# Optimization experiments

Measured on AMD Instinct MI355X. Metric: run time of the kernel, lower is better.

## Reference

```python
import jax, jax.numpy as jnp
import numpy as np

# Config constants (match init_kwargs)
E = 32          # num_experts
K = 4           # num_experts_per_token
G = 4           # num_expert_group
TG = 2          # topk_group
H = 2048        # hidden_size
F = 1024        # moe_intermediate_size
FS = 2048       # shared expert intermediate (moe_intermediate_size * num_shared_experts)
SCALE = 2.0     # routed_scaling_factor
B, S = 2, 1024
N = B * S
CAP = 2 * (N * K // E)


def setup_inputs() -> dict:
    key = jax.random.key(0)
    ks = jax.random.split(key, 9)
    w = 0.02  # init scale for weights
    return {
        "hidden_states": jax.random.normal(ks[0], (B, S, H), jnp.float32),
        "gate_w": jax.random.normal(ks[1], (E, H), jnp.float32) * w,
        "gate_bias": jax.random.normal(ks[2], (E,), jnp.float32) * w,
        "w1": jax.random.normal(ks[3], (E, H, F), jnp.float32) * w,
        "w2": jax.random.normal(ks[4], (E, F, H), jnp.float32) * w,
        "w3": jax.random.normal(ks[5], (E, H, F), jnp.float32) * w,
        "shared_gate": jax.random.normal(ks[6], (H, FS), jnp.float32) * w,
        "shared_up": jax.random.normal(ks[7], (H, FS), jnp.float32) * w,
        "shared_down": jax.random.normal(ks[8], (FS, H), jnp.float32) * w,
    }


def _gate(x, gate_w, gate_bias):
    # x: [N, H] -> (topk_idx [N,K] int32, topk_w [N,K] f32)
    logits = x @ gate_w.T                       # [N, E]
    scores = jax.nn.sigmoid(logits)
    sc = scores + gate_bias                     # scores_for_choice
    n = x.shape[0]
    grp = sc.reshape(n, G, E // G)
    group_scores = jax.lax.top_k(grp, 2)[0].sum(-1)          # [N, G]
    _, gidx = jax.lax.top_k(group_scores, TG)                # [N, TG]
    gmask = jnp.zeros((n, G), sc.dtype).at[jnp.arange(n)[:, None], gidx].set(1.0)
    smask = jnp.repeat(gmask, E // G, axis=1)                # [N, E]
    tmp = jnp.where(smask > 0, sc, 0.0)
    _, topk_idx = jax.lax.top_k(tmp, K)                      # [N, K]
    topk_w = jnp.take_along_axis(scores, topk_idx, axis=1)
    topk_w = topk_w / (topk_w.sum(-1, keepdims=True) + 1e-20)  # renormalize (K>1)
    return topk_idx, topk_w * SCALE


def _moe(x, topk_idx, topk_w, w1, w2, w3):
    # Capacity-based dispatch -> grouped SwiGLU GEMMs -> weighted combine.
    n = x.shape[0]
    flat_e = topk_idx.reshape(-1)                            # [N*K]
    oh = jax.nn.one_hot(flat_e, E, dtype=jnp.int32)
    pos = (jnp.cumsum(oh, axis=0) * oh).sum(-1) - 1          # slot within expert
    keep = pos < CAP
    slot = jnp.where(keep, pos, CAP)                         # CAP -> dropped via mode='drop'
    x_rep = jnp.repeat(x, K, axis=0)                         # [N*K, H]
    buf = jnp.zeros((E, CAP, H), x.dtype).at[flat_e, slot].set(x_rep, mode='drop')
    h = jax.nn.silu(jnp.einsum('ech,ehf->ecf', buf, w1)) * jnp.einsum('ech,ehf->ecf', buf, w3)
    ob = jnp.einsum('ecf,efh->ech', h, w2)                   # [E, CAP, H]
    y = ob[flat_e, jnp.minimum(slot, CAP - 1)]               # [N*K, H]
    y = jnp.where(keep[:, None], y, 0.0)
    return (y.reshape(n, K, H) * topk_w[:, :, None]).sum(1)  # [N, H]


def reference(hidden_states, gate_w, gate_bias, w1, w2, w3, shared_gate, shared_up, shared_down):
    b, s, h = hidden_states.shape
    x = hidden_states.reshape(-1, h)
    topk_idx, topk_w = _gate(x, gate_w, gate_bias)
    out = _moe(x, topk_idx, topk_w, w1, w2, w3)
    shared = (jax.nn.silu(x @ shared_gate) * (x @ shared_up)) @ shared_down
    return (out + shared).reshape(b, s, h)
```

## Files before the change

### kernel.cpp

```cpp
#include <hip/hip_runtime.h>
#include <stdint.h>
#include <math.h>

#define NTOK 2048
#define HDIM 2048
#define FDIM 1024
#define NEXP 32
#define TOPK 4
#define NGRP 4
#define CAP  512

typedef _Float16 f16;
typedef _Float16 half8 __attribute__((ext_vector_type(8)));
typedef float f32x4 __attribute__((ext_vector_type(4)));

__device__ __forceinline__ int swz3(int n) { return (n ^ (n >> 2)) & 3; }

__global__ __launch_bounds__(256) void gateconv_kernel(const float* __restrict__ x,
                                                       const float* __restrict__ gw,
                                                       const float* __restrict__ gb,
                                                       int* __restrict__ tidx,
                                                       float* __restrict__ tw,
                                                       f16* __restrict__ xbt) {
  int t = blockIdx.x;
  int tid = threadIdx.x;
  int e = tid >> 3, p = tid & 7;
  const f32x4* xr = (const f32x4*)(x + (size_t)t * HDIM);
  const f32x4* wr = (const f32x4*)(gw + (size_t)e * HDIM);
  float s = 0.f;
  for (int c = 0; c < 64; c++) {
    f32x4 a = xr[p + c * 8], w = wr[p + c * 8];
    s += a[0] * w[0] + a[1] * w[1] + a[2] * w[2] + a[3] * w[3];
  }
  s += __shfl_down(s, 4, 8);
  s += __shfl_down(s, 2, 8);
  s += __shfl_down(s, 1, 8);
  __shared__ float lg[NEXP];
  if (p == 0) lg[e] = s;

  {
    int c8 = tid * 8;
    const float* pp = x + (size_t)t * HDIM + c8;
    f32x4 a = *(const f32x4*)pp;
    f32x4 b = *(const f32x4*)(pp + 4);
    half8 v;
    v[0] = (f16)a[0]; v[1] = (f16)a[1]; v[2] = (f16)a[2]; v[3] = (f16)a[3];
    v[4] = (f16)b[0]; v[5] = (f16)b[1]; v[6] = (f16)b[2]; v[7] = (f16)b[3];
    *(half8*)((char*)xbt + (size_t)(c8 >> 5) * 131072 + t * 64 + (c8 & 31) * 2) = v;
  }

  __syncthreads();
  if (tid == 0) {
    float sc[NEXP], scb[NEXP];
    for (int i = 0; i < NEXP; i++) {
      sc[i] = 1.f / (1.f + expf(-lg[i]));
      scb[i] = sc[i] + gb[i];
    }
    float gs[NGRP];
    for (int g = 0; g < NGRP; g++) {
      float m1 = -1e30f, m2 = -1e30f;
      for (int j = 0; j < 8; j++) {
        float v = scb[g * 8 + j];
        if (v > m1) { m2 = m1; m1 = v; }
        else if (v > m2) m2 = v;
      }
      gs[g] = m1 + m2;
    }
    int g1 = 0; float bv = gs[0];
    for (int g = 1; g < NGRP; g++) if (gs[g] > bv) { bv = gs[g]; g1 = g; }
    int g2 = -1; bv = -1e30f;
    for (int g = 0; g < NGRP; g++) if (g != g1 && gs[g] > bv) { bv = gs[g]; g2 = g; }
    float cand[NEXP];
    for (int i = 0; i < NEXP; i++) {
      int g = i >> 3;
      cand[i] = (g == g1 || g == g2) ? scb[i] : 0.0f;
    }
    int isel[TOPK]; float wsel[TOPK]; float wsum = 0.f;
    bool used[NEXP] = {};
    for (int k = 0; k < TOPK; k++) {
      int best = 0; float bw = -1e30f;
      for (int i = 0; i < NEXP; i++)
        if (!used[i] && cand[i] > bw) { bw = cand[i]; best = i; }
      used[best] = true;
      isel[k] = best;
      wsel[k] = sc[best];
      wsum += wsel[k];
    }
    float inv = 2.0f / (wsum + 1e-20f);
    for (int k = 0; k < TOPK; k++) {
      tidx[t * TOPK + k] = isel[k];
      tw[t * TOPK + k] = wsel[k] * inv;
    }
  }
}

__global__ __launch_bounds__(256) void dispatch_kernel(const int* __restrict__ tidx,
                                                       const float* __restrict__ tw,
                                                       int* __restrict__ tok,
                                                       float* __restrict__ wt,
                                                       int* __restrict__ cnt) {
  int e = blockIdx.x, tid = threadIdx.x, wv = tid >> 6, lane = tid & 63;
  __shared__ int wsum[4];
  __shared__ int sbase;
  if (tid == 0) sbase = 0;
  __syncthreads();
  for (int c = 0; c < (NTOK * TOPK) / 256; c++) {
    int i = c * 256 + tid;
    int fe = tidx[i];
    bool flag = (fe == e);
    unsigned long long b = __ballot(flag ? 1 : 0);
    int lr = __popcll(b & ((1ull << lane) - 1ull));
    if (lane == 0) wsum[wv] = __popcll(b);
    __syncthreads();
    int off = 0;
    for (int w2 = 0; w2 < wv; w2++) off += wsum[w2];
    int tot = wsum[0] + wsum[1] + wsum[2] + wsum[3];
    int base = sbase;
    if (flag) {
      int pos = base + off + lr;
      if (pos < CAP) {
        tok[e * CAP + pos] = i >> 2;
        wt[e * CAP + pos] = tw[i];
      }
    }
    __syncthreads();
    if (tid == 0) sbase = base + tot;
  }
  __syncthreads();
  if (tid == 0) cnt[e] = min(sbase, CAP);
}

__global__ __launch_bounds__(256) void gather_kernel(const f16* __restrict__ xbt,
                                                     const int* __restrict__ tok,
                                                     const int* __restrict__ cnt,
                                                     f16* __restrict__ xg) {
  int bid = blockIdx.x;
  int t = bid & 63, e = bid >> 6;
  int cn = cnt[e];
  int tid = threadIdx.x;
  char* dst = (char*)xg + (size_t)e * 2097152 + (size_t)t * 32768;
  const char* srcb = (const char*)xbt + (size_t)t * 131072;
  for (int s = tid; s < cn; s += 256) {
    const uint4* sp = (const uint4*)(srcb + (size_t)tok[e * CAP + s] * 64);
    uint4 v0 = sp[0], v1 = sp[1], v2 = sp[2], v3 = sp[3];
    uint4* dp = (uint4*)(dst + s * 64);
    dp[0] = v0; dp[1] = v1; dp[2] = v2; dp[3] = v3;
  }
}

template<int MODE>
__device__ void gemm_body(int bid, const f16* __restrict__ Ag, const float* __restrict__ B0g,
                          const float* __restrict__ B1g, void* __restrict__ outp,
                          const int* __restrict__ tokL, const float* __restrict__ wtL,
                          const int* __restrict__ cntP, char* bs) {
  constexpr int BM = (MODE == 0 || MODE == 2) ? 512 : 256;
  constexpr int BN = (MODE == 2) ? 64 : 32;
  constexpr bool DUAL = (MODE <= 1);
  constexpr int MF = BM / 64;
  constexpr int NF = BN / 16;
  constexpr int KD = (MODE == 2) ? 1024 : 2048;
  constexpr int NK = KD / 32;
  constexpr int ND = (MODE == 0) ? 1024 : 2048;
  constexpr size_t TS = (MODE == 0 || MODE == 2) ? 32768 : 131072;
  constexpr int BSZ = (DUAL ? 2 : 1) * BN * 64;

  int tid = threadIdx.x, lane = tid & 63, wv = tid >> 6;
  int e = 0, m0 = 0, n0 = 0;
  if constexpr (MODE == 0 || MODE == 2) {
    e = (bid & 7) + ((bid >> 3) >> 5) * 8;
    n0 = ((bid >> 3) & 31) * BN;
  } else {
    n0 = ((bid & 7) * 8 + ((bid >> 3) & 7)) * 32;
    m0 = ((bid >> 3) >> 3) * 256;
  }

  const char* Ab = (const char*)Ag;
  const float* B0 = B0g;
  const float* B1 = B1g;
  int Mcur = 0;
  if constexpr (MODE == 0 || MODE == 2) {
    Mcur = cntP[e];
    Ab += (size_t)e * ((MODE == 0) ? 2097152 : 1048576);
    B0 += (size_t)e * ((size_t)KD * ND);
    if constexpr (MODE == 0) B1 += (size_t)e * ((size_t)KD * ND);
  }

  int kb = tid >> 3;
  int nbL = (tid & 7) * (BN / 8);

  unsigned voff[MF];
#pragma unroll
  for (int mf = 0; mf < MF; mf++) {
    int row = ((MODE == 0 || MODE == 2) ? (wv * (BM / 4)) : (m0 + wv * 64)) + mf * 16 + (lane & 15);
    voff[mf] = row * 64 + ((lane >> 4) << 4);
  }

  f32x4 acc0[MF][NF];
  f32x4 acc1[DUAL ? MF : 1][DUAL ? NF : 1];
#pragma unroll
  for (int mf = 0; mf < MF; mf++)
#pragma unroll
    for (int nf = 0; nf < NF; nf++) acc0[mf][nf] = (f32x4){0.f, 0.f, 0.f, 0.f};
  if constexpr (DUAL) {
#pragma unroll
    for (int mf = 0; mf < MF; mf++)
#pragma unroll
      for (int nf = 0; nf < NF; nf++) acc1[mf][nf] = (f32x4){0.f, 0.f, 0.f, 0.f};
  }

  half8 af[MF];
  half8 bf0[NF];
  half8 bf1[DUAL ? NF : 1];
  f32x4 bE0, bE1, bO0, bO1;

  auto loadB = [&](int t, f32x4& X, f32x4& Y) {
    const float* s = B0 + (size_t)(t * 32 + kb) * ND + n0 + nbL;
    X = *(const f32x4*)s;
    if constexpr (DUAL) {
      Y = *(const f32x4*)(B1 + (size_t)(t * 32 + kb) * ND + n0 + nbL);
    } else if constexpr (MODE == 2) {
      Y = *(const f32x4*)(s + 4);
    }
  };
  auto writeB = [&](const f32x4& X, const f32x4& Y, int par) {
    char* base = bs + par * BSZ;
#pragma unroll
    for (int q = 0; q < 4; q++) {
      int n = nbL + q;
      int off = n * 64 + (((kb >> 3) ^ swz3(n)) << 4) + (kb & 7) * 2;
      *(f16*)(base + off) = (f16)X[q];
      if constexpr (DUAL) {
        *(f16*)(base + BN * 64 + off) = (f16)Y[q];
      } else if constexpr (MODE == 2) {
        int n2 = n + 4;
        int off2 = n2 * 64 + (((kb >> 3) ^ swz3(n2)) << 4) + (kb & 7) * 2;
        *(f16*)(base + off2) = (f16)Y[q];
      }
    }
  };
  auto bfread = [&](int par) {
#pragma unroll
    for (int nf = 0; nf < NF; nf++) {
      int n = nf * 16 + (lane & 15);
      int off = par * BSZ + n * 64 + (((lane >> 4) ^ swz3(n)) << 4);
      bf0[nf] = *(const half8*)(bs + off);
      if constexpr (DUAL) bf1[nf] = *(const half8*)(bs + BN * 64 + off);
    }
  };
  auto loadAf = [&](int t) {
#pragma unroll
    for (int mf = 0; mf < MF; mf++)
      af[mf] = *(const half8*)(Ab + (size_t)t * TS + voff[mf]);
  };
  auto domfma = [&]() {
#pragma unroll
    for (int mf = 0; mf < MF; mf++)
#pragma unroll
      for (int nf = 0; nf < NF; nf++) {
        acc0[mf][nf] = __builtin_amdgcn_mfma_f32_16x16x32_f16(af[mf], bf0[nf], acc0[mf][nf], 0, 0, 0);
        if constexpr (DUAL)
          acc1[mf][nf] = __builtin_amdgcn_mfma_f32_16x16x32_f16(af[mf], bf1[nf], acc1[mf][nf], 0, 0, 0);
      }
  };

  loadB(0, bE0, bE1);
  loadB(1, bO0, bO1);
  loadAf(0);
  writeB(bE0, bE1, 0);
  asm volatile("s_waitcnt lgkmcnt(0)" ::: "memory");
  __builtin_amdgcn_s_barrier();

  for (int t = 0; t < NK; t += 2) {
    bfread(0);
    writeB(bO0, bO1, 1);
    if (t + 2 < NK) loadB(t + 2, bE0, bE1);
    domfma();
    loadAf(t + 1 < NK ? t + 1 : t);
    asm volatile("s_waitcnt lgkmcnt(0)" ::: "memory");
    __builtin_amdgcn_s_barrier();
    bfread(1);
    if (t + 2 < NK) writeB(bE0, bE1, 0);
    if (t + 3 < NK) loadB(t + 3, bO0, bO1);
    domfma();
    if (t + 2 < NK) {
      loadAf(t + 2);
      asm volatile("s_waitcnt lgkmcnt(0)" ::: "memory");
      __builtin_amdgcn_s_barrier();
    }
  }

  int koff = (lane >> 4) << 2;
  if constexpr (MODE == 0) {
    char* Hb = (char*)outp + (size_t)e * 1048576;
#pragma unroll
    for (int mf = 0; mf < MF; mf++)
#pragma unroll
      for (int j = 0; j < 4; j++) {
        int slot = wv * 128 + mf * 16 + koff + j;
        if (slot < Mcur) {
#pragma unroll
          for (int nf = 0; nf < NF; nf++) {
            int col = n0 + nf * 16 + (lane & 15);
            float g = acc0[mf][nf][j], u = acc1[mf][nf][j];
            float val = g / (1.f + expf(-g)) * u;
            *(f16*)(Hb + (size_t)(col >> 5) * 32768 + slot * 64 + (col & 31) * 2) = (f16)val;
          }
        }
      }
  } else if constexpr (MODE == 1) {
    char* Hb = (char*)outp;
#pragma unroll
    for (int mf = 0; mf < MF; mf++)
#pragma unroll
      for (int j = 0; j < 4; j++) {
        int row = m0 + wv * 64 + mf * 16 + koff + j;
#pragma unroll
        for (int nf = 0; nf < NF; nf++) {
          int col = n0 + nf * 16 + (lane & 15);
          float g = acc0[mf][nf][j], u = acc1[mf][nf][j];
          float val = g / (1.f + expf(-g)) * u;
          *(f16*)(Hb + (size_t)(col >> 5) * 131072 + row * 64 + (col & 31) * 2) = (f16)val;
        }
      }
  } else if constexpr (MODE == 2) {
    float* Of = (float*)outp;
    const int* tokp = tokL + e * CAP;
    const float* wtp = wtL + e * CAP;
#pragma unroll
    for (int mf = 0; mf < MF; mf++)
#pragma unroll
      for (int j = 0; j < 4; j++) {
        int slot = wv * 128 + mf * 16 + koff + j;
        if (slot < Mcur) {
          int tk = tokp[slot];
          float w = wtp[slot];
#pragma unroll
          for (int nf = 0; nf < NF; nf++) {
            int col = n0 + nf * 16 + (lane & 15);
            atomicAdd(Of + (size_t)tk * HDIM + col, acc0[mf][nf][j] * w);
          }
        }
      }
  } else {
    float* Of = (float*)outp;
#pragma unroll
    for (int mf = 0; mf < MF; mf++)
#pragma unroll
      for (int j = 0; j < 4; j++) {
        int row = m0 + wv * 64 + mf * 16 + koff + j;
#pragma unroll
        for (int nf = 0; nf < NF; nf++) {
          int col = n0 + nf * 16 + (lane & 15);
          atomicAdd(Of + (size_t)row * HDIM + col, acc0[mf][nf][j]);
        }
      }
  }
}

__global__ __launch_bounds__(256, 2) void fused_up_kernel(
    const f16* __restrict__ xg, const f16* __restrict__ xbt,
    const float* __restrict__ w1, const float* __restrict__ w3,
    const float* __restrict__ sg, const float* __restrict__ su,
    void* __restrict__ hbuf, void* __restrict__ hs, const int* __restrict__ cnt) {
  __shared__ __align__(16) char bs[8192];
  int bid = blockIdx.x;
  if (bid < 1024) gemm_body<0>(bid, xg, w1, w3, hbuf, nullptr, nullptr, cnt, bs);
  else            gemm_body<1>(bid - 1024, xbt, sg, su, hs, nullptr, nullptr, nullptr, bs);
}

__global__ __launch_bounds__(256, 2) void fused_down_kernel(
    const f16* __restrict__ hbuf, const f16* __restrict__ hs,
    const float* __restrict__ w2, const float* __restrict__ sd,
    float* __restrict__ out, const int* __restrict__ tok,
    const float* __restrict__ wt, const int* __restrict__ cnt) {
  __shared__ __align__(16) char bs[8192];
  int bid = blockIdx.x;
  if (bid < 1024) gemm_body<2>(bid, hbuf, w2, nullptr, out, tok, wt, cnt, bs);
  else            gemm_body<3>(bid - 1024, hs, sd, nullptr, out, nullptr, nullptr, nullptr, bs);
}

extern "C" void kernel_launch(void* const* d_in, const int* in_sizes, int n_in,
                              void* d_out, int out_size, void* d_ws, size_t ws_size,
                              hipStream_t stream) {
  const float* x  = (const float*)d_in[0];
  const float* gw = (const float*)d_in[1];
  const float* gb = (const float*)d_in[2];
  const float* w1 = (const float*)d_in[3];
  const float* w2 = (const float*)d_in[4];
  const float* w3 = (const float*)d_in[5];
  const float* sg = (const float*)d_in[6];
  const float* su = (const float*)d_in[7];
  const float* sd = (const float*)d_in[8];
  float* out = (float*)d_out;
  char* ws = (char*)d_ws;

  f16*   xbt = (f16*)(ws);
  f16*   hs  = (f16*)(ws + 8388608);
  f16*   hbuf= (f16*)(ws + 16777216);
  f16*   xg  = (f16*)(ws + 50331648);
  int*   tok = (int*)(ws + 117440512);
  float* wt  = (float*)(ws + 117506048);
  int*   tidx= (int*)(ws + 117571584);
  float* tw  = (float*)(ws + 117604352);
  int*   cnt = (int*)(ws + 117637120);

  gateconv_kernel<<<2048, 256, 0, stream>>>(x, gw, gb, tidx, tw, xbt);
  dispatch_kernel<<<32, 256, 0, stream>>>(tidx, tw, tok, wt, cnt);
  gather_kernel<<<2048, 256, 0, stream>>>(xbt, tok, cnt, xg);

  fused_up_kernel<<<1536, 256, 0, stream>>>(xg, xbt, w1, w3, sg, su, hbuf, hs, cnt);

  hipMemsetAsync(out, 0, (size_t)out_size * sizeof(float), stream);
  fused_down_kernel<<<1536, 256, 0, stream>>>(hbuf, hs, w2, sd, out, tok, wt, cnt);
}
```

Baseline: 545.4 us.

## Switch to 128x128 square GEMM tiles with compact expert packing and separate SwiGLU pass

Replaces the tall-skinny per-expert GEMM tiles (512x32/64) with a shared 128x128 core using a 2x2 wave layout. The goal is to raise reuse of both A and B per block and to cut redundant fp32 weight loads. Expert rows are now packed compactly through a prefix-sum offset kernel, and empty M tiles return early. The gate and up projections are written separately to fp16 buffers and combined by a new elementwise SwiGLU kernel, which adds extra memory traffic and two launches in exchange for the tiling change.

Result: no change. 548.9 us (+0.6%).

```diff
diff --git a/kernel.cpp b/kernel.cpp
--- a/kernel.cpp
+++ b/kernel.cpp
@@ -12,6 +12,7 @@
 
 typedef _Float16 f16;
 typedef _Float16 half8 __attribute__((ext_vector_type(8)));
+typedef _Float16 half2v __attribute__((ext_vector_type(2)));
 typedef float f32x4 __attribute__((ext_vector_type(4)));
 
 __device__ __forceinline__ int swz3(int n) { return (n ^ (n >> 2)) & 3; }
@@ -130,15 +131,23 @@
   if (tid == 0) cnt[e] = min(sbase, CAP);
 }
 
+__global__ void scan_kernel(const int* __restrict__ cnt, int* __restrict__ offs) {
+  if (threadIdx.x == 0) {
+    int s = 0;
+    for (int e = 0; e < NEXP; e++) { offs[e] = s; s += cnt[e]; }
+  }
+}
+
 __global__ __launch_bounds__(256) void gather_kernel(const f16* __restrict__ xbt,
                                                      const int* __restrict__ tok,
                                                      const int* __restrict__ cnt,
+                                                     const int* __restrict__ offs,
                                                      f16* __restrict__ xg) {
   int bid = blockIdx.x;
   int t = bid & 63, e = bid >> 6;
   int cn = cnt[e];
   int tid = threadIdx.x;
-  char* dst = (char*)xg + (size_t)e * 2097152 + (size_t)t * 32768;
+  char* dst = (char*)xg + (size_t)offs[e] * 4096 + (size_t)t * cn * 64;
   const char* srcb = (const char*)xbt + (size_t)t * 131072;
   for (int s = tid; s < cn; s += 256) {
     const uint4* sp = (const uint4*)(srcb + (size_t)tok[e * CAP + s] * 64);
@@ -148,235 +157,235 @@
   }
 }
 
-template<int MODE>
-__device__ void gemm_body(int bid, const f16* __restrict__ Ag, const float* __restrict__ B0g,
-                          const float* __restrict__ B1g, void* __restrict__ outp,
-                          const int* __restrict__ tokL, const float* __restrict__ wtL,
-                          const int* __restrict__ cntP, char* bs) {
-  constexpr int BM = (MODE == 0 || MODE == 2) ? 512 : 256;
-  constexpr int BN = (MODE == 2) ? 64 : 32;
-  constexpr bool DUAL = (MODE <= 1);
-  constexpr int MF = BM / 64;
-  constexpr int NF = BN / 16;
-  constexpr int KD = (MODE == 2) ? 1024 : 2048;
-  constexpr int NK = KD / 32;
-  constexpr int ND = (MODE == 0) ? 1024 : 2048;
-  constexpr size_t TS = (MODE == 0 || MODE == 2) ? 32768 : 131072;
-  constexpr int BSZ = (DUAL ? 2 : 1) * BN * 64;
-
+#define SYNC() { asm volatile("s_waitcnt lgkmcnt(0)" ::: "memory"); __builtin_amdgcn_s_barrier(); }
+
+__device__ __forceinline__ void core128(const char* __restrict__ Ab, int tsA, int NKt,
+                                        const float* __restrict__ Bb, int ND,
+                                        char* lds, f32x4 (&acc)[4][4]) {
   int tid = threadIdx.x, lane = tid & 63, wv = tid >> 6;
-  int e = 0, m0 = 0, n0 = 0;
-  if constexpr (MODE == 0 || MODE == 2) {
-    e = (bid & 7) + ((bid >> 3) >> 5) * 8;
-    n0 = ((bid >> 3) & 31) * BN;
-  } else {
-    n0 = ((bid & 7) * 8 + ((bid >> 3) & 7)) * 32;
-    m0 = ((bid >> 3) >> 3) * 256;
-  }
-
-  const char* Ab = (const char*)Ag;
-  const float* B0 = B0g;
-  const float* B1 = B1g;
-  int Mcur = 0;
-  if constexpr (MODE == 0 || MODE == 2) {
-    Mcur = cntP[e];
-    Ab += (size_t)e * ((MODE == 0) ? 2097152 : 1048576);
-    B0 += (size_t)e * ((size_t)KD * ND);
-    if constexpr (MODE == 0) B1 += (size_t)e * ((size_t)KD * ND);
-  }
-
-  int kb = tid >> 3;
-  int nbL = (tid & 7) * (BN / 8);
-
-  unsigned voff[MF];
-#pragma unroll
-  for (int mf = 0; mf < MF; mf++) {
-    int row = ((MODE == 0 || MODE == 2) ? (wv * (BM / 4)) : (m0 + wv * 64)) + mf * 16 + (lane & 15);
-    voff[mf] = row * 64 + ((lane >> 4) << 4);
-  }
-
-  f32x4 acc0[MF][NF];
-  f32x4 acc1[DUAL ? MF : 1][DUAL ? NF : 1];
-#pragma unroll
-  for (int mf = 0; mf < MF; mf++)
-#pragma unroll
-    for (int nf = 0; nf < NF; nf++) acc0[mf][nf] = (f32x4){0.f, 0.f, 0.f, 0.f};
-  if constexpr (DUAL) {
-#pragma unroll
-    for (int mf = 0; mf < MF; mf++)
-#pragma unroll
-      for (int nf = 0; nf < NF; nf++) acc1[mf][nf] = (f32x4){0.f, 0.f, 0.f, 0.f};
-  }
-
-  half8 af[MF];
-  half8 bf0[NF];
-  half8 bf1[DUAL ? NF : 1];
-  f32x4 bE0, bE1, bO0, bO1;
-
-  auto loadB = [&](int t, f32x4& X, f32x4& Y) {
-    const float* s = B0 + (size_t)(t * 32 + kb) * ND + n0 + nbL;
-    X = *(const f32x4*)s;
-    if constexpr (DUAL) {
-      Y = *(const f32x4*)(B1 + (size_t)(t * 32 + kb) * ND + n0 + nbL);
-    } else if constexpr (MODE == 2) {
-      Y = *(const f32x4*)(s + 4);
-    }
-  };
-  auto writeB = [&](const f32x4& X, const f32x4& Y, int par) {
-    char* base = bs + par * BSZ;
-#pragma unroll
-    for (int q = 0; q < 4; q++) {
-      int n = nbL + q;
-      int off = n * 64 + (((kb >> 3) ^ swz3(n)) << 4) + (kb & 7) * 2;
-      *(f16*)(base + off) = (f16)X[q];
-      if constexpr (DUAL) {
-        *(f16*)(base + BN * 64 + off) = (f16)Y[q];
-      } else if constexpr (MODE == 2) {
-        int n2 = n + 4;
-        int off2 = n2 * 64 + (((kb >> 3) ^ swz3(n2)) << 4) + (kb & 7) * 2;
-        *(f16*)(base + off2) = (f16)Y[q];
-      }
-    }
-  };
-  auto bfread = [&](int par) {
-#pragma unroll
-    for (int nf = 0; nf < NF; nf++) {
-      int n = nf * 16 + (lane & 15);
-      int off = par * BSZ + n * 64 + (((lane >> 4) ^ swz3(n)) << 4);
-      bf0[nf] = *(const half8*)(bs + off);
-      if constexpr (DUAL) bf1[nf] = *(const half8*)(bs + BN * 64 + off);
-    }
-  };
-  auto loadAf = [&](int t) {
-#pragma unroll
-    for (int mf = 0; mf < MF; mf++)
-      af[mf] = *(const half8*)(Ab + (size_t)t * TS + voff[mf]);
-  };
-  auto domfma = [&]() {
-#pragma unroll
-    for (int mf = 0; mf < MF; mf++)
-#pragma unroll
-      for (int nf = 0; nf < NF; nf++) {
-        acc0[mf][nf] = __builtin_amdgcn_mfma_f32_16x16x32_f16(af[mf], bf0[nf], acc0[mf][nf], 0, 0, 0);
-        if constexpr (DUAL)
-          acc1[mf][nf] = __builtin_amdgcn_mfma_f32_16x16x32_f16(af[mf], bf1[nf], acc1[mf][nf], 0, 0, 0);
-      }
-  };
-
-  loadB(0, bE0, bE1);
-  loadB(1, bO0, bO1);
-  loadAf(0);
-  writeB(bE0, bE1, 0);
-  asm volatile("s_waitcnt lgkmcnt(0)" ::: "memory");
-  __builtin_amdgcn_s_barrier();
-
-  for (int t = 0; t < NK; t += 2) {
-    bfread(0);
-    writeB(bO0, bO1, 1);
-    if (t + 2 < NK) loadB(t + 2, bE0, bE1);
-    domfma();
-    loadAf(t + 1 < NK ? t + 1 : t);
-    asm volatile("s_waitcnt lgkmcnt(0)" ::: "memory");
-    __builtin_amdgcn_s_barrier();
-    bfread(1);
-    if (t + 2 < NK) writeB(bE0, bE1, 0);
-    if (t + 3 < NK) loadB(t + 3, bO0, bO1);
-    domfma();
-    if (t + 2 < NK) {
-      loadAf(t + 2);
-      asm volatile("s_waitcnt lgkmcnt(0)" ::: "memory");
-      __builtin_amdgcn_s_barrier();
-    }
-  }
-
-  int koff = (lane >> 4) << 2;
-  if constexpr (MODE == 0) {
-    char* Hb = (char*)outp + (size_t)e * 1048576;
-#pragma unroll
-    for (int mf = 0; mf < MF; mf++)
-#pragma unroll
-      for (int j = 0; j < 4; j++) {
-        int slot = wv * 128 + mf * 16 + koff + j;
-        if (slot < Mcur) {
-#pragma unroll
-          for (int nf = 0; nf < NF; nf++) {
-            int col = n0 + nf * 16 + (lane & 15);
-            float g = acc0[mf][nf][j], u = acc1[mf][nf][j];
-            float val = g / (1.f + expf(-g)) * u;
-            *(f16*)(Hb + (size_t)(col >> 5) * 32768 + slot * 64 + (col & 31) * 2) = (f16)val;
-          }
-        }
-      }
-  } else if constexpr (MODE == 1) {
-    char* Hb = (char*)outp;
-#pragma unroll
-    for (int mf = 0; mf < MF; mf++)
-#pragma unroll
-      for (int j = 0; j < 4; j++) {
-        int row = m0 + wv * 64 + mf * 16 + koff + j;
-#pragma unroll
-        for (int nf = 0; nf < NF; nf++) {
-          int col = n0 + nf * 16 + (lane & 15);
-          float g = acc0[mf][nf][j], u = acc1[mf][nf][j];
-          float val = g / (1.f + expf(-g)) * u;
-          *(f16*)(Hb + (size_t)(col >> 5) * 131072 + row * 64 + (col & 31) * 2) = (f16)val;
-        }
-      }
-  } else if constexpr (MODE == 2) {
-    float* Of = (float*)outp;
-    const int* tokp = tokL + e * CAP;
-    const float* wtp = wtL + e * CAP;
-#pragma unroll
-    for (int mf = 0; mf < MF; mf++)
-#pragma unroll
-      for (int j = 0; j < 4; j++) {
-        int slot = wv * 128 + mf * 16 + koff + j;
-        if (slot < Mcur) {
-          int tk = tokp[slot];
-          float w = wtp[slot];
-#pragma unroll
-          for (int nf = 0; nf < NF; nf++) {
-            int col = n0 + nf * 16 + (lane & 15);
-            atomicAdd(Of + (size_t)tk * HDIM + col, acc0[mf][nf][j] * w);
-          }
-        }
-      }
-  } else {
-    float* Of = (float*)outp;
-#pragma unroll
-    for (int mf = 0; mf < MF; mf++)
-#pragma unroll
-      for (int j = 0; j < 4; j++) {
-        int row = m0 + wv * 64 + mf * 16 + koff + j;
-#pragma unroll
-        for (int nf = 0; nf < NF; nf++) {
-          int col = n0 + nf * 16 + (lane & 15);
-          atomicAdd(Of + (size_t)row * HDIM + col, acc0[mf][nf][j]);
-        }
-      }
-  }
+  int wn = (wv & 1) * 64;
+  int wm = (wv >> 1) * 64;
+  int kgrp = (tid >> 5) * 2;
+  int n4 = (tid & 31) * 4;
+  const float* B0r = Bb + (size_t)kgrp * ND + n4;
+  const float* B1r = Bb + (size_t)(kgrp + 16) * ND + n4;
+
+  unsigned aoff[4];
+#pragma unroll
+  for (int mf = 0; mf < 4; mf++)
+    aoff[mf] = (wm + mf * 16 + (lane & 15)) * 64 + ((lane >> 4) << 4);
+
+  int wo0[4], wo1[4];
+#pragma unroll
+  for (int q = 0; q < 4; q++) {
+    int n = n4 + q;
+    wo0[q] = n * 64 + ((((kgrp) >> 3) ^ swz3(n)) << 4) + (kgrp & 7) * 2;
+    wo1[q] = n * 64 + ((((kgrp + 16) >> 3) ^ swz3(n)) << 4) + (kgrp & 7) * 2;
+  }
+
+  half8 afA[4], afB[4], bf[4];
+  f32x4 E0, E1, E2, E3, O0, O1, O2, O3;
+
+#define LOADB(tt, S0, S1, S2, S3) { size_t _o = (size_t)(tt) * 32 * ND; \
+    S0 = *(const f32x4*)(B0r + _o); S1 = *(const f32x4*)(B0r + _o + ND); \
+    S2 = *(const f32x4*)(B1r + _o); S3 = *(const f32x4*)(B1r + _o + ND); }
+
+#define WRITEB(S0, S1, S2, S3, par) { char* _b = lds + (par) * 8192; \
+    _Pragma("unroll") for (int _q = 0; _q < 4; _q++) { \
+      half2v _h0; _h0[0] = (f16)S0[_q]; _h0[1] = (f16)S1[_q]; \
+      *(half2v*)(_b + wo0[_q]) = _h0; \
+      half2v _h1; _h1[0] = (f16)S2[_q]; _h1[1] = (f16)S3[_q]; \
+      *(half2v*)(_b + wo1[_q]) = _h1; } }
+
+#define BFREAD(par) { _Pragma("unroll") for (int _f = 0; _f < 4; _f++) { \
+      int _n = wn + _f * 16 + (lane & 15); \
+      bf[_f] = *(const half8*)(lds + (par) * 8192 + _n * 64 + (((lane >> 4) ^ swz3(_n)) << 4)); } }
+
+#define LOADA(tt, AF) { _Pragma("unroll") for (int _m = 0; _m < 4; _m++) \
+      AF[_m] = *(const half8*)(Ab + (size_t)(tt) * tsA + aoff[_m]); }
+
+#define DOMFMA(AF) { _Pragma("unroll") for (int _m = 0; _m < 4; _m++) \
+      _Pragma("unroll") for (int _f = 0; _f < 4; _f++) \
+        acc[_m][_f] = __builtin_amdgcn_mfma_f32_16x16x32_f16(AF[_m], bf[_f], acc[_m][_f], 0, 0, 0); }
+
+  LOADB(0, E0, E1, E2, E3)
+  LOADB(1, O0, O1, O2, O3)
+  WRITEB(E0, E1, E2, E3, 0)
+  LOADA(0, afA)
+  SYNC()
+
+  for (int t = 0; t < NKt; t += 2) {
+    BFREAD(0)
+    LOADA(t + 1, afB)
+    WRITEB(O0, O1, O2, O3, 1)
+    if (t + 2 < NKt) LOADB(t + 2, E0, E1, E2, E3)
+    DOMFMA(afA)
+    SYNC()
+    BFREAD(1)
+    if (t + 2 < NKt) {
+      LOADA(t + 2, afA)
+      WRITEB(E0, E1, E2, E3, 0)
+      if (t + 3 < NKt) LOADB(t + 3, O0, O1, O2, O3)
+    }
+    DOMFMA(afB)
+    if (t + 2 < NKt) SYNC()
+  }
+
+#undef LOADB
+#undef WRITEB
+#undef BFREAD
+#undef LOADA
+#undef DOMFMA
 }
 
 __global__ __launch_bounds__(256, 2) void fused_up_kernel(
     const f16* __restrict__ xg, const f16* __restrict__ xbt,
     const float* __restrict__ w1, const float* __restrict__ w3,
     const float* __restrict__ sg, const float* __restrict__ su,
-    void* __restrict__ hbuf, void* __restrict__ hs, const int* __restrict__ cnt) {
-  __shared__ __align__(16) char bs[8192];
+    f16* __restrict__ hg, f16* __restrict__ hu,
+    f16* __restrict__ hsg, f16* __restrict__ hsu,
+    const int* __restrict__ cnt, const int* __restrict__ offs) {
+  __shared__ __align__(16) char lds[16384];
   int bid = blockIdx.x;
-  if (bid < 1024) gemm_body<0>(bid, xg, w1, w3, hbuf, nullptr, nullptr, cnt, bs);
-  else            gemm_body<1>(bid - 1024, xbt, sg, su, hs, nullptr, nullptr, nullptr, bs);
+  int tid = threadIdx.x, lane = tid & 63, wv = tid >> 6;
+  int wm = (wv >> 1) * 64, wn = (wv & 1) * 64, koff = (lane >> 4) << 2;
+
+  f32x4 acc[4][4];
+#pragma unroll
+  for (int mf = 0; mf < 4; mf++)
+#pragma unroll
+    for (int nf = 0; nf < 4; nf++) acc[mf][nf] = (f32x4){0.f, 0.f, 0.f, 0.f};
+
+  if (bid < 2048) {
+    int elo = bid & 7, n = (bid >> 3) & 7, m = (bid >> 6) & 3, ehi = (bid >> 8) & 3, mat = bid >> 10;
+    int e = elo + ehi * 8;
+    int ce = cnt[e];
+    int m0 = m * 128;
+    if (m0 >= ce) return;
+    int oe = offs[e];
+    const char* Ab = (const char*)xg + (size_t)oe * 4096 + m0 * 64;
+    const float* B = (mat ? w3 : w1) + (size_t)e * 2048 * 1024 + n * 128;
+    core128(Ab, ce * 64, 64, B, 1024, lds, acc);
+    char* Hb = (char*)(mat ? hu : hg) + (size_t)oe * 2048;
+    size_t kts = (size_t)ce * 64;
+#pragma unroll
+    for (int mf = 0; mf < 4; mf++)
+#pragma unroll
+      for (int j = 0; j < 4; j++) {
+        int gs = m0 + wm + mf * 16 + koff + j;
+        if (gs < ce) {
+#pragma unroll
+          for (int nf = 0; nf < 4; nf++) {
+            int gc = n * 128 + wn + nf * 16 + (lane & 15);
+            *(f16*)(Hb + (size_t)(gc >> 5) * kts + gs * 64 + (gc & 31) * 2) = (f16)acc[mf][nf][j];
+          }
+        }
+      }
+  } else {
+    int b2 = bid - 2048;
+    int mat = b2 >> 8, rem = b2 & 255, m = rem >> 4, n = rem & 15;
+    int m0 = m * 128;
+    const char* Ab = (const char*)xbt + m0 * 64;
+    const float* B = (mat ? su : sg) + n * 128;
+    core128(Ab, 131072, 64, B, 2048, lds, acc);
+    char* Hb = (char*)(mat ? hsu : hsg);
+#pragma unroll
+    for (int mf = 0; mf < 4; mf++)
+#pragma unroll
+      for (int j = 0; j < 4; j++) {
+        int gs = m0 + wm + mf * 16 + koff + j;
+#pragma unroll
+        for (int nf = 0; nf < 4; nf++) {
+          int gc = n * 128 + wn + nf * 16 + (lane & 15);
+          *(f16*)(Hb + (size_t)(gc >> 5) * 131072 + gs * 64 + (gc & 31) * 2) = (f16)acc[mf][nf][j];
+        }
+      }
+  }
+}
+
+__global__ __launch_bounds__(256) void combine_kernel(
+    const f16* __restrict__ hg, const f16* __restrict__ hu, f16* __restrict__ hbuf,
+    const f16* __restrict__ hsg, const f16* __restrict__ hsu, f16* __restrict__ hs) {
+  size_t i = ((size_t)blockIdx.x * 256 + threadIdx.x) * 8;
+  const f16 *gp, *up;
+  f16* op;
+  if (i < 8388608) { gp = hg + i; up = hu + i; op = hbuf + i; }
+  else { size_t j = i - 8388608; gp = hsg + j; up = hsu + j; op = hs + j; }
+  half8 g = *(const half8*)gp;
+  half8 u = *(const half8*)up;
+  half8 o;
+#pragma unroll
+  for (int k = 0; k < 8; k++) {
+    float gv = (float)g[k];
+    float uv = (float)u[k];
+    o[k] = (f16)(gv / (1.f + expf(-gv)) * uv);
+  }
+  *(half8*)op = o;
 }
 
 __global__ __launch_bounds__(256, 2) void fused_down_kernel(
     const f16* __restrict__ hbuf, const f16* __restrict__ hs,
     const float* __restrict__ w2, const float* __restrict__ sd,
     float* __restrict__ out, const int* __restrict__ tok,
-    const float* __restrict__ wt, const int* __restrict__ cnt) {
-  __shared__ __align__(16) char bs[8192];
+    const float* __restrict__ wt, const int* __restrict__ cnt,
+    const int* __restrict__ offs) {
+  __shared__ __align__(16) char lds[16384];
   int bid = blockIdx.x;
-  if (bid < 1024) gemm_body<2>(bid, hbuf, w2, nullptr, out, tok, wt, cnt, bs);
-  else            gemm_body<3>(bid - 1024, hs, sd, nullptr, out, nullptr, nullptr, nullptr, bs);
+  int tid = threadIdx.x, lane = tid & 63, wv = tid >> 6;
+  int wm = (wv >> 1) * 64, wn = (wv & 1) * 64, koff = (lane >> 4) << 2;
+
+  f32x4 acc[4][4];
+#pragma unroll
+  for (int mf = 0; mf < 4; mf++)
+#pragma unroll
+    for (int nf = 0; nf < 4; nf++) acc[mf][nf] = (f32x4){0.f, 0.f, 0.f, 0.f};
+
+  if (bid < 2048) {
+    int elo = bid & 7, n = (bid >> 3) & 15, m = (bid >> 7) & 3, ehi = (bid >> 9) & 3;
+    int e = elo + ehi * 8;
+    int ce = cnt[e];
+    int m0 = m * 128;
+    if (m0 >= ce) return;
+    int oe = offs[e];
+    const char* Ab = (const char*)hbuf + (size_t)oe * 2048 + m0 * 64;
+    const float* B = w2 + (size_t)e * 1024 * 2048 + n * 128;
+    core128(Ab, ce * 64, 32, B, 2048, lds, acc);
+    const int* tokp = tok + e * CAP;
+    const float* wtp = wt + e * CAP;
+#pragma unroll
+    for (int mf = 0; mf < 4; mf++)
+#pragma unroll
+      for (int j = 0; j < 4; j++) {
+        int gs = m0 + wm + mf * 16 + koff + j;
+        if (gs < ce) {
+          int tk = tokp[gs];
+          float w = wtp[gs];
+#pragma unroll
+          for (int nf = 0; nf < 4; nf++) {
+            int gc = n * 128 + wn + nf * 16 + (lane & 15);
+            atomicAdd(out + (size_t)tk * HDIM + gc, acc[mf][nf][j] * w);
+          }
+        }
+      }
+  } else {
+    int b2 = bid - 2048;
+    int m = b2 >> 4, n = b2 & 15;
+    int m0 = m * 128;
+    const char* Ab = (const char*)hs + m0 * 64;
+    const float* B = sd + n * 128;
+    core128(Ab, 131072, 64, B, 2048, lds, acc);
+#pragma unroll
+    for (int mf = 0; mf < 4; mf++)
+#pragma unroll
+      for (int j = 0; j < 4; j++) {
+        int gs = m0 + wm + mf * 16 + koff + j;
+#pragma unroll
+        for (int nf = 0; nf < 4; nf++) {
+          int gc = n * 128 + wn + nf * 16 + (lane & 15);
+          atomicAdd(out + (size_t)gs * HDIM + gc, acc[mf][nf][j]);
+        }
+      }
+  }
 }
 
 extern "C" void kernel_launch(void* const* d_in, const int* in_sizes, int n_in,
@@ -394,22 +403,30 @@
   float* out = (float*)d_out;
   char* ws = (char*)d_ws;
 
-  f16*   xbt = (f16*)(ws);
-  f16*   hs  = (f16*)(ws + 8388608);
-  f16*   hbuf= (f16*)(ws + 16777216);
-  f16*   xg  = (f16*)(ws + 50331648);
-  int*   tok = (int*)(ws + 117440512);
-  float* wt  = (float*)(ws + 117506048);
-  int*   tidx= (int*)(ws + 117571584);
-  float* tw  = (float*)(ws + 117604352);
-  int*   cnt = (int*)(ws + 117637120);
+  f16*   xbt  = (f16*)(ws);
+  f16*   hsg  = (f16*)(ws + 8388608);
+  f16*   hsu  = (f16*)(ws + 16777216);
+  f16*   hs   = (f16*)(ws + 25165824);
+  f16*   hg   = (f16*)(ws + 33554432);
+  f16*   hu   = (f16*)(ws + 50331648);
+  f16*   xg   = (f16*)(ws + 67108864);
+  f16*   hbuf = (f16*)(ws + 67108864);
+  int*   tok  = (int*)(ws + 101711872);
+  float* wt   = (float*)(ws + 101777408);
+  int*   tidx = (int*)(ws + 101842944);
+  float* tw   = (float*)(ws + 101875712);
+  int*   cnt  = (int*)(ws + 101908480);
+  int*   offs = (int*)(ws + 101908608);
 
   gateconv_kernel<<<2048, 256, 0, stream>>>(x, gw, gb, tidx, tw, xbt);
   dispatch_kernel<<<32, 256, 0, stream>>>(tidx, tw, tok, wt, cnt);
-  gather_kernel<<<2048, 256, 0, stream>>>(xbt, tok, cnt, xg);
-
-  fused_up_kernel<<<1536, 256, 0, stream>>>(xg, xbt, w1, w3, sg, su, hbuf, hs, cnt);
+  scan_kernel<<<1, 32, 0, stream>>>(cnt, offs);
+  gather_kernel<<<2048, 256, 0, stream>>>(xbt, tok, cnt, offs, xg);
+
+  fused_up_kernel<<<2560, 256, 0, stream>>>(xg, xbt, w1, w3, sg, su,
+                                            hg, hu, hsg, hsu, cnt, offs);
+  combine_kernel<<<6144, 256, 0, stream>>>(hg, hu, hbuf, hsg, hsu, hs);
 
   hipMemsetAsync(out, 0, (size_t)out_size * sizeof(float), stream);
-  fused_down_kernel<<<1536, 256, 0, stream>>>(hbuf, hs, w2, sd, out, tok, wt, cnt);
-}
+  fused_down_kernel<<<2304, 256, 0, stream>>>(hbuf, hs, w2, sd, out, tok, wt, cnt, offs);
+}
```
